# Kernel optimization log

Hardware: AMD Instinct MI355X
Metric: run time of the kernel (lower is better)

The kernel has to match this reference:

```python
import jax, jax.numpy as jnp
import numpy as np

D = 32       # hidden_size (hardcoded in AR.__init__)
H = 16       # num_heads
HD = D // H  # head_dim = 2
L = 8        # num DiT blocks
MLP = 128    # mlp_ratio 4.0
B, S, T, P = 16, 1024, 256, 32
SCALE = float(1.0 / np.sqrt(HD))


def _ln(x, g, b, eps=1e-6):
    mu = jnp.mean(x, axis=-1, keepdims=True)
    var = jnp.mean((x - mu) ** 2, axis=-1, keepdims=True)
    return (x - mu) * jax.lax.rsqrt(var + eps) * g + b


def _mha(q_in, kv_in, in_w, in_b, out_w, out_b):
    # nn.MultiheadAttention math, batch-first layout (permutation-equivalent)
    wq, wk, wv = in_w[:D], in_w[D:2 * D], in_w[2 * D:]
    bq, bk, bv = in_b[:D], in_b[D:2 * D], in_b[2 * D:]
    Bq, Sq = q_in.shape[0], q_in.shape[1]
    Sk = kv_in.shape[1]
    q = (q_in @ wq.T + bq).reshape(Bq, Sq, H, HD)
    k = (kv_in @ wk.T + bk).reshape(Bq, Sk, H, HD)
    v = (kv_in @ wv.T + bv).reshape(Bq, Sk, H, HD)
    scores = jnp.einsum('bqhd,bkhd->bhqk', q, k) * SCALE
    a = jax.nn.softmax(scores, axis=-1)
    o = jnp.einsum('bhqk,bkhd->bqhd', a, v).reshape(Bq, Sq, D)
    return o @ out_w.T + out_b


def setup_inputs() -> dict:
    key = jax.random.key(0)
    ks = iter(jax.random.split(key, 40))
    rn = lambda k, sh, sc=1.0: jax.random.normal(k, sh, jnp.float32) * sc
    inp = {
        'x': rn(next(ks), (B, S, D)),
        'speaker_emb': rn(next(ks), (B, P, D)),
        'text_phonemes': rn(next(ks), (B, T, D)),
        'timestep_emb': rn(next(ks), (B, D)),
        'mask': jnp.ones((S,), jnp.float32),
        # per-block params, stacked over L for lax.scan
        'ln1_g': jnp.ones((L, D)), 'ln1_b': jnp.zeros((L, D)),
        'ln2_g': jnp.ones((L, D)), 'ln2_b': jnp.zeros((L, D)),
        'ln22_g': jnp.ones((L, D)), 'ln22_b': jnp.zeros((L, D)),
        'ln3_g': jnp.ones((L, D)), 'ln3_b': jnp.zeros((L, D)),
        'attn_in_w': rn(next(ks), (L, 3 * D, D), 0.1), 'attn_in_b': jnp.zeros((L, 3 * D)),
        'attn_out_w': rn(next(ks), (L, D, D), 0.1), 'attn_out_b': jnp.zeros((L, D)),
        'cross_in_w': rn(next(ks), (L, 3 * D, D), 0.1), 'cross_in_b': jnp.zeros((L, 3 * D)),
        'cross_out_w': rn(next(ks), (L, D, D), 0.1), 'cross_out_b': jnp.zeros((L, D)),
        'ts_w': rn(next(ks), (L, 2 * D, D), 0.1), 'ts_b': jnp.zeros((L, 2 * D)),
        'fc1_w': rn(next(ks), (L, MLP, D), 0.1), 'fc1_b': jnp.zeros((L, MLP)),
        'fc2_w': rn(next(ks), (L, D, MLP), 0.1), 'fc2_b': jnp.zeros((L, D)),
    }
    return inp


def _forward(x, speaker_emb, text_phonemes, timestep_emb, mask, params):
    m = mask[None, :, None]  # (1, S, 1), matches mask.unsqueeze(0).unsqueeze(2)
    def body(h, p):
        h = h * m
        hn = _ln(h, p['ln1_g'], p['ln1_b'])
        h = h + _mha(hn, hn, p['attn_in_w'], p['attn_in_b'], p['attn_out_w'], p['attn_out_b'])
        # both cross attentions use cross_attn weights (cross_attn2 is dead code in source)
        ca1 = _mha(_ln(h, p['ln2_g'], p['ln2_b']), text_phonemes,
                   p['cross_in_w'], p['cross_in_b'], p['cross_out_w'], p['cross_out_b'])
        ca2 = _mha(_ln(h, p['ln22_g'], p['ln22_b']), speaker_emb,
                   p['cross_in_w'], p['cross_in_b'], p['cross_out_w'], p['cross_out_b'])
        h = h + ca1 + ca2
        ss = timestep_emb @ p['ts_w'].T + p['ts_b']        # (B, 2D)
        scale, shift = ss[:, :D], ss[:, D:]
        hm = _ln(h, p['ln3_g'], p['ln3_b']) * (1.0 + scale[:, None, :]) + shift[:, None, :]
        mlp = jax.nn.gelu(hm @ p['fc1_w'].T + p['fc1_b'], approximate=False) @ p['fc2_w'].T + p['fc2_b']
        return (h + mlp) * m, None
    out, _ = jax.lax.scan(body, x, params)
    return out


def reference(x, speaker_emb, text_phonemes, timestep_emb, mask,
              ln1_g, ln1_b, ln2_g, ln2_b, ln22_g, ln22_b, ln3_g, ln3_b,
              attn_in_w, attn_in_b, attn_out_w, attn_out_b,
              cross_in_w, cross_in_b, cross_out_w, cross_out_b,
              ts_w, ts_b, fc1_w, fc1_b, fc2_w, fc2_b):
    params = dict(ln1_g=ln1_g, ln1_b=ln1_b, ln2_g=ln2_g, ln2_b=ln2_b,
                  ln22_g=ln22_g, ln22_b=ln22_b, ln3_g=ln3_g, ln3_b=ln3_b,
                  attn_in_w=attn_in_w, attn_in_b=attn_in_b,
                  attn_out_w=attn_out_w, attn_out_b=attn_out_b,
                  cross_in_w=cross_in_w, cross_in_b=cross_in_b,
                  cross_out_w=cross_out_w, cross_out_b=cross_out_b,
                  ts_w=ts_w, ts_b=ts_b, fc1_w=fc1_w, fc1_b=fc1_b,
                  fc2_w=fc2_w, fc2_b=fc2_b)
    return _forward(x, speaker_emb, text_phonemes, timestep_emb, mask, params)
```

## Files before the change

kernel.cpp:

```cpp
#include <hip/hip_runtime.h>
#include <math.h>

#define NB 16
#define SEQ 1024
#define NT 16384
#define TT 256
#define PP 32
#define NL 8
#define SCALE 0.70710678118654752f
#define LOG2E 1.4426950408889634f
#define CS (SCALE * LOG2E)

static __device__ __forceinline__ float exp2fast(float x) {
#if __has_builtin(__builtin_amdgcn_exp2f)
  return __builtin_amdgcn_exp2f(x);
#else
  return exp2f(x);
#endif
}

__global__ __launch_bounds__(256) void k_pre(const float* __restrict__ tse,
                                             const float* __restrict__ tsw,
                                             const float* __restrict__ tsb,
                                             float* __restrict__ ssa,
                                             const float* __restrict__ text,
                                             const float* __restrict__ spk,
                                             const float* __restrict__ cw,
                                             const float* __restrict__ cb,
                                             float* __restrict__ kvtT,
                                             float* __restrict__ kvsT) {
  __shared__ float sh[64 * 33];
  int tid = threadIdx.x;
  int bx = blockIdx.x;
  if (bx < 32) {
    int idx = bx * 256 + tid;
    int l = idx >> 10;
    int rem = idx & 1023;
    int b = rem >> 6;
    int j = rem & 63;
    const float* wr = tsw + ((size_t)l * 64 + j) * 32;
    const float* xr = tse + b * 32;
    float acc = tsb[l * 64 + j];
#pragma unroll
    for (int e = 0; e < 32; e++) acc = fmaf(xr[e], wr[e], acc);
    ssa[idx] = acc;
    return;
  }
  const float* src;
  float* dst;
  int l, tok0, ntok;
  if (bx < 544) {
    l = (bx - 32) >> 6; tok0 = ((bx - 32) & 63) * 64; ntok = NB * TT; src = text;
    dst = kvtT + (size_t)l * 64 * ntok;
  } else {
    l = (bx - 544) >> 3; tok0 = ((bx - 544) & 7) * 64; ntok = NB * PP; src = spk;
    dst = kvsT + (size_t)l * 64 * ntok;
  }
  const float* w = cw + (size_t)l * 96 * 32 + 32 * 32;
  const float* wb = cb + (size_t)l * 96 + 32;
  for (int i = tid; i < 64 * 32; i += 256) {
    int tl = i >> 5, e = i & 31;
    sh[tl * 33 + e] = src[(size_t)(tok0 + tl) * 32 + e];
  }
  __syncthreads();
  int tl = tid & 63;
  int wv = tid >> 6;
#pragma unroll
  for (int k = 0; k < 16; k++) {
    int j = __builtin_amdgcn_readfirstlane(wv + 4 * k);
    const float* wr = w + j * 32;
    const float* hr = sh + tl * 33;
    float acc = wb[j];
#pragma unroll
    for (int e = 0; e < 32; e++) acc = fmaf(hr[e], wr[e], acc);
    dst[(size_t)j * ntok + tok0 + tl] = acc;
  }
}

__device__ __forceinline__ void load_row32(const float* __restrict__ base, int tok, float* r) {
#pragma unroll
  for (int e = 0; e < 32; e++) r[e] = base[(size_t)e * NT + tok];
}

__device__ __forceinline__ void ln_core(float* r) {
  float a0 = 0, a1 = 0, a2 = 0, a3 = 0;
#pragma unroll
  for (int e = 0; e < 32; e += 4) { a0 += r[e]; a1 += r[e + 1]; a2 += r[e + 2]; a3 += r[e + 3]; }
  float mu = ((a0 + a1) + (a2 + a3)) * (1.0f / 32.0f);
  float v0 = 0, v1 = 0, v2 = 0, v3 = 0;
#pragma unroll
  for (int e = 0; e < 32; e += 4) {
    float d0 = r[e] - mu, d1 = r[e + 1] - mu, d2 = r[e + 2] - mu, d3 = r[e + 3] - mu;
    v0 = fmaf(d0, d0, v0); v1 = fmaf(d1, d1, v1); v2 = fmaf(d2, d2, v2); v3 = fmaf(d3, d3, v3);
  }
  float rstd = rsqrtf(((v0 + v1) + (v2 + v3)) * (1.0f / 32.0f) + 1e-6f);
#pragma unroll
  for (int e = 0; e < 32; e++) r[e] = (r[e] - mu) * rstd;
}

__global__ __launch_bounds__(256) void k_qkv(const float* __restrict__ hin,
                                             int rowmajor,
                                             float* __restrict__ hT,
                                             const float* __restrict__ mask,
                                             const float* __restrict__ w,
                                             const float* __restrict__ wb,
                                             const float* __restrict__ g,
                                             const float* __restrict__ bv,
                                             float* __restrict__ qkvT) {
  int tid = threadIdx.x;
  int tok0 = blockIdx.x * 64;
  int yc = blockIdx.y;
  int tl = tid & 63, wv = tid >> 6;
  int tok = tok0 + tl;
  float r[32];
  if (rowmajor) {
    float m = mask[tok & (SEQ - 1)];
#pragma unroll
    for (int e = 0; e < 32; e++) r[e] = hin[(size_t)tok * 32 + e] * m;
    if (yc == 0 && wv == 0) {
#pragma unroll
      for (int e = 0; e < 32; e++) hT[(size_t)e * NT + tok] = r[e];
    }
  } else {
    load_row32(hin, tok, r);
  }
  ln_core(r);
#pragma unroll
  for (int e = 0; e < 32; e++) r[e] = fmaf(r[e], g[e], bv[e]);
#pragma unroll
  for (int k = 0; k < 6; k++) {
    int j = __builtin_amdgcn_readfirstlane(yc * 24 + wv + 4 * k);
    const float* wr = w + j * 32;
    float acc = wb[j];
#pragma unroll
    for (int e = 0; e < 32; e++) acc = fmaf(r[e], wr[e], acc);
    qkvT[(size_t)j * NT + tok] = acc;
  }
}

__global__ __launch_bounds__(256) void k_projq12(const float* __restrict__ hA,
                                                 const float* __restrict__ oT,
                                                 const float* __restrict__ aow,
                                                 const float* __restrict__ aob,
                                                 float* __restrict__ hB,
                                                 const float* __restrict__ cwq,
                                                 const float* __restrict__ cbq,
                                                 const float* __restrict__ g2, const float* __restrict__ b2,
                                                 const float* __restrict__ g22, const float* __restrict__ b22,
                                                 float* __restrict__ q1T,
                                                 float* __restrict__ q2T) {
  __shared__ float sh[32 * 33];
  __shared__ float so[32 * 33];
  int tid = threadIdx.x;
  int tok0 = blockIdx.x * 32;
  int y = blockIdx.y;
  for (int i = tid; i < 1024; i += 256) {
    int e = i >> 5, t = i & 31;
    sh[t * 33 + e] = hA[(size_t)e * NT + tok0 + t];
    so[t * 33 + e] = oT[(size_t)e * NT + tok0 + t];
  }
  __syncthreads();
  int tl = tid & 31, jg = tid >> 5;
#pragma unroll
  for (int kk = 0; kk < 4; kk++) {
    int j = jg + 8 * kk;
    const float* wr = aow + j * 32;
    float acc = aob[j];
#pragma unroll
    for (int i = 0; i < 32; i++) acc = fmaf(so[tl * 33 + i], wr[i], acc);
    float hp = sh[tl * 33 + j] + acc;
    sh[tl * 33 + j] = hp;
    if (y == 0) hB[(size_t)j * NT + tok0 + tl] = hp;
  }
  __syncthreads();
  float r[32];
#pragma unroll
  for (int i = 0; i < 32; i++) r[i] = sh[tl * 33 + i];
  ln_core(r);
  const float* g = y ? g22 : g2;
  const float* bb = y ? b22 : b2;
  float* dst = y ? q2T : q1T;
#pragma unroll
  for (int i = 0; i < 32; i++) r[i] = fmaf(r[i], g[i], bb[i]);
#pragma unroll
  for (int kk = 0; kk < 4; kk++) {
    int j = jg + 8 * kk;
    const float* wr = cwq + j * 32;
    float acc = cbq[j];
#pragma unroll
    for (int i = 0; i < 32; i++) acc = fmaf(r[i], wr[i], acc);
    dst[(size_t)j * NT + tok0 + tl] = acc;
  }
}

__global__ __launch_bounds__(256) void k_projfc1(const float* __restrict__ hBp,
                                                 const float* __restrict__ o1T,
                                                 const float* __restrict__ o2T,
                                                 const float* __restrict__ cow,
                                                 const float* __restrict__ cob,
                                                 float* __restrict__ hC,
                                                 const float* __restrict__ ssl,
                                                 const float* __restrict__ g3, const float* __restrict__ b3,
                                                 const float* __restrict__ w1, const float* __restrict__ b1,
                                                 float* __restrict__ uT) {
  __shared__ float sh[32 * 33];
  __shared__ float so[32 * 33];
  int tid = threadIdx.x;
  int tok0 = blockIdx.x * 32;
  int yc = blockIdx.y;
  for (int i = tid; i < 1024; i += 256) {
    int e = i >> 5, t = i & 31;
    sh[t * 33 + e] = hBp[(size_t)e * NT + tok0 + t];
    so[t * 33 + e] = o1T[(size_t)e * NT + tok0 + t] + o2T[(size_t)e * NT + tok0 + t];
  }
  __syncthreads();
  int tl = tid & 31, jg = tid >> 5;
#pragma unroll
  for (int kk = 0; kk < 4; kk++) {
    int j = jg + 8 * kk;
    const float* wr = cow + j * 32;
    float acc = 2.0f * cob[j];
#pragma unroll
    for (int i = 0; i < 32; i++) acc = fmaf(so[tl * 33 + i], wr[i], acc);
    float hp = sh[tl * 33 + j] + acc;
    sh[tl * 33 + j] = hp;
    if (yc == 0) hC[(size_t)j * NT + tok0 + tl] = hp;
  }
  __syncthreads();
  float r[32];
#pragma unroll
  for (int i = 0; i < 32; i++) r[i] = sh[tl * 33 + i];
  ln_core(r);
  int b = tok0 >> 10;
  const float* sc = ssl + b * 64;
#pragma unroll
  for (int i = 0; i < 32; i++) {
    float ln = fmaf(r[i], g3[i], b3[i]);
    r[i] = fmaf(ln, 1.0f + sc[i], sc[32 + i]);
  }
#pragma unroll
  for (int kk = 0; kk < 4; kk++) {
    int j = yc * 32 + jg + 8 * kk;
    const float* wr = w1 + j * 32;
    float acc = b1[j];
#pragma unroll
    for (int i = 0; i < 32; i++) acc = fmaf(r[i], wr[i], acc);
    float ge = 0.5f * acc * (1.0f + erff(acc * 0.70710678118654752f));
    uT[(size_t)j * NT + tok0 + tl] = ge;
  }
}

template <int SK, int SETS>
__device__ __forceinline__ void attn_core(const float* __restrict__ qb,
                                          const float* __restrict__ kb,
                                          const float* __restrict__ vb,
                                          int kvld,
                                          float* __restrict__ ob) {
  constexpr int RPW = 4 * SETS;
  constexpr int RPB = 4 * RPW;
  constexpr int NRC = SEQ / RPB;
  int tid = threadIdx.x;
  int bx = blockIdx.x;
  int rc = bx % NRC, bh = bx / NRC;
  int b = bh >> 4, hh = bh & 15;
  int wv = tid >> 6, lane = tid & 63;
  int rg = lane >> 4, kl = lane & 15;
  int rbase = rc * RPB + wv * RPW + rg;

  const float* qxp = qb + (size_t)(2 * hh) * NT + b * SEQ;
  const float* qyp = qxp + NT;
  const float* kx = kb + (size_t)(2 * hh) * kvld + b * SK;
  const float* ky = kx + kvld;
  const float* vx = vb + (size_t)(2 * hh) * kvld + b * SK;
  const float* vy = vx + kvld;

  float qx[SETS], qy[SETS], sum[SETS], ox[SETS], oy[SETS];
#pragma unroll
  for (int s = 0; s < SETS; s++) {
    qx[s] = qxp[rbase + 4 * s] * CS;
    qy[s] = qyp[rbase + 4 * s] * CS;
    sum[s] = 0.f; ox[s] = 0.f; oy[s] = 0.f;
  }

  if constexpr (SK >= 64) {
    const float4* kx4 = (const float4*)(kx + kl * 4);
    const float4* ky4 = (const float4*)(ky + kl * 4);
    const float4* vx4 = (const float4*)(vx + kl * 4);
    const float4* vy4 = (const float4*)(vy + kl * 4);
#pragma unroll 4
    for (int c = 0; c < SK / 64; c++) {
      float4 k4x = kx4[c * 16];
      float4 k4y = ky4[c * 16];
      float4 v4x = vx4[c * 16];
      float4 v4y = vy4[c * 16];
#pragma unroll
      for (int s = 0; s < SETS; s++) {
        float e0 = exp2fast(fmaf(qy[s], k4y.x, qx[s] * k4x.x));
        float e1 = exp2fast(fmaf(qy[s], k4y.y, qx[s] * k4x.y));
        float e2 = exp2fast(fmaf(qy[s], k4y.z, qx[s] * k4x.z));
        float e3 = exp2fast(fmaf(qy[s], k4y.w, qx[s] * k4x.w));
        sum[s] += (e0 + e1) + (e2 + e3);
        ox[s] = fmaf(e0, v4x.x, ox[s]);
        ox[s] = fmaf(e1, v4x.y, ox[s]);
        ox[s] = fmaf(e2, v4x.z, ox[s]);
        ox[s] = fmaf(e3, v4x.w, ox[s]);
        oy[s] = fmaf(e0, v4y.x, oy[s]);
        oy[s] = fmaf(e1, v4y.y, oy[s]);
        oy[s] = fmaf(e2, v4y.z, oy[s]);
        oy[s] = fmaf(e3, v4y.w, oy[s]);
      }
    }
  } else {
    float2 k2x = *(const float2*)(kx + kl * 2);
    float2 k2y = *(const float2*)(ky + kl * 2);
    float2 v2x = *(const float2*)(vx + kl * 2);
    float2 v2y = *(const float2*)(vy + kl * 2);
#pragma unroll
    for (int s = 0; s < SETS; s++) {
      float e0 = exp2fast(fmaf(qy[s], k2y.x, qx[s] * k2x.x));
      float e1 = exp2fast(fmaf(qy[s], k2y.y, qx[s] * k2x.y));
      sum[s] += e0 + e1;
      ox[s] = fmaf(e0, v2x.x, ox[s]);
      ox[s] = fmaf(e1, v2x.y, ox[s]);
      oy[s] = fmaf(e0, v2y.x, oy[s]);
      oy[s] = fmaf(e1, v2y.y, oy[s]);
    }
  }

  float* oxr = ob + (size_t)(2 * hh) * NT + b * SEQ;
  float* oyr = oxr + NT;
#pragma unroll
  for (int s = 0; s < SETS; s++) {
    float sm = sum[s];
    float o1 = ox[s];
    float o2 = oy[s];
#pragma unroll
    for (int off = 1; off < 16; off <<= 1) {
      sm += __shfl_xor(sm, off);
      o1 += __shfl_xor(o1, off);
      o2 += __shfl_xor(o2, off);
    }
    if (kl == 0) {
      float inv = 1.0f / sm;
      int r = rbase + 4 * s;
      oxr[r] = o1 * inv;
      oyr[r] = o2 * inv;
    }
  }
}

__global__ __launch_bounds__(256) void k_attn_self(const float* __restrict__ qkvT,
                                                   float* __restrict__ oT) {
  attn_core<SEQ, 8>(qkvT, qkvT + (size_t)32 * NT, qkvT + (size_t)64 * NT, NT, oT);
}

__global__ __launch_bounds__(256) void k_attn_cross(const float* __restrict__ q1T,
                                                    const float* __restrict__ q2T,
                                                    const float* __restrict__ kvt,
                                                    const float* __restrict__ kvs,
                                                    float* __restrict__ o1T,
                                                    float* __restrict__ o2T) {
  if (blockIdx.y == 0)
    attn_core<TT, 8>(q1T, kvt, kvt + (size_t)32 * (NB * TT), NB * TT, o1T);
  else
    attn_core<PP, 8>(q2T, kvs, kvs + (size_t)32 * (NB * PP), NB * PP, o2T);
}

__global__ __launch_bounds__(256) void k_fc2(const float* __restrict__ uT,
                                             float* hT,
                                             float* __restrict__ out_rm,
                                             const float* __restrict__ mask,
                                             const float* __restrict__ w2,
                                             const float* __restrict__ b2) {
  __shared__ __align__(16) float shu[64 * 132];
  int tid = threadIdx.x;
  int tok0 = blockIdx.x * 64, yc = blockIdx.y;
  for (int i = tid; i < 64 * 128; i += 256) {
    int e = i >> 6, tl = i & 63;
    shu[tl * 132 + e] = uT[(size_t)e * NT + tok0 + tl];
  }
  __syncthreads();
  int tl = tid & 63, wv = tid >> 6;
  int tok = tok0 + tl;
  int j0 = __builtin_amdgcn_readfirstlane(yc * 16 + wv);
  int j1 = __builtin_amdgcn_readfirstlane(j0 + 4);
  int j2 = __builtin_amdgcn_readfirstlane(j0 + 8);
  int j3 = __builtin_amdgcn_readfirstlane(j0 + 12);
  const float* w0 = w2 + j0 * 128;
  const float* w1 = w2 + j1 * 128;
  const float* w2r = w2 + j2 * 128;
  const float* w3 = w2 + j3 * 128;
  float a0 = b2[j0], a1 = b2[j1], a2 = b2[j2], a3 = b2[j3];
  const float4* ur = (const float4*)(shu + tl * 132);
#pragma unroll
  for (int m = 0; m < 32; m++) {
    float4 t = ur[m];
    a0 = fmaf(t.x, w0[4 * m], a0); a0 = fmaf(t.y, w0[4 * m + 1], a0);
    a0 = fmaf(t.z, w0[4 * m + 2], a0); a0 = fmaf(t.w, w0[4 * m + 3], a0);
    a1 = fmaf(t.x, w1[4 * m], a1); a1 = fmaf(t.y, w1[4 * m + 1], a1);
    a1 = fmaf(t.z, w1[4 * m + 2], a1); a1 = fmaf(t.w, w1[4 * m + 3], a1);
    a2 = fmaf(t.x, w2r[4 * m], a2); a2 = fmaf(t.y, w2r[4 * m + 1], a2);
    a2 = fmaf(t.z, w2r[4 * m + 2], a2); a2 = fmaf(t.w, w2r[4 * m + 3], a2);
    a3 = fmaf(t.x, w3[4 * m], a3); a3 = fmaf(t.y, w3[4 * m + 1], a3);
    a3 = fmaf(t.z, w3[4 * m + 2], a3); a3 = fmaf(t.w, w3[4 * m + 3], a3);
  }
  float mk = mask[tok & (SEQ - 1)];
  size_t g0 = (size_t)j0 * NT + tok, g1 = (size_t)j1 * NT + tok;
  size_t g2i = (size_t)j2 * NT + tok, g3 = (size_t)j3 * NT + tok;
  float r0 = (hT[g0] + a0) * mk;
  float r1 = (hT[g1] + a1) * mk;
  float r2 = (hT[g2i] + a2) * mk;
  float r3 = (hT[g3] + a3) * mk;
  if (out_rm) {
    out_rm[(size_t)tok * 32 + j0] = r0;
    out_rm[(size_t)tok * 32 + j1] = r1;
    out_rm[(size_t)tok * 32 + j2] = r2;
    out_rm[(size_t)tok * 32 + j3] = r3;
  } else {
    hT[g0] = r0;
    hT[g1] = r1;
    hT[g2i] = r2;
    hT[g3] = r3;
  }
}

extern "C" void kernel_launch(void* const* d_in, const int* in_sizes, int n_in,
                              void* d_out, int out_size, void* d_ws, size_t ws_size,
                              hipStream_t stream) {
  const float* x = (const float*)d_in[0];
  const float* spk = (const float*)d_in[1];
  const float* text = (const float*)d_in[2];
  const float* tse = (const float*)d_in[3];
  const float* mask = (const float*)d_in[4];
  const float* ln1_g = (const float*)d_in[5];
  const float* ln1_b = (const float*)d_in[6];
  const float* ln2_g = (const float*)d_in[7];
  const float* ln2_b = (const float*)d_in[8];
  const float* ln22_g = (const float*)d_in[9];
  const float* ln22_b = (const float*)d_in[10];
  const float* ln3_g = (const float*)d_in[11];
  const float* ln3_b = (const float*)d_in[12];
  const float* aw = (const float*)d_in[13];
  const float* ab = (const float*)d_in[14];
  const float* aow = (const float*)d_in[15];
  const float* aob = (const float*)d_in[16];
  const float* cw = (const float*)d_in[17];
  const float* cb = (const float*)d_in[18];
  const float* cow = (const float*)d_in[19];
  const float* cob = (const float*)d_in[20];
  const float* tsw = (const float*)d_in[21];
  const float* tsb = (const float*)d_in[22];
  const float* f1w = (const float*)d_in[23];
  const float* f1b = (const float*)d_in[24];
  const float* f2w = (const float*)d_in[25];
  const float* f2b = (const float*)d_in[26];

  float* ws = (float*)d_ws;
  const size_t SL = (size_t)32 * NT;
  float* hS = ws;
  float* qkvT = ws + SL;
  float* q1T = ws + 2 * SL;
  float* q2T = ws + 3 * SL;
  float* oS = ws + 4 * SL;
  float* hB = ws + SL;
  float* o1c = ws + 6 * SL;
  float* o2c = ws + 7 * SL;
  float* uT = ws + 2 * SL;
  float* kvtT = ws + 8 * SL;
  float* kvsT = kvtT + (size_t)NL * 64 * (NB * TT);
  float* ssa = kvsT + (size_t)NL * 64 * (NB * PP);

  k_pre<<<608, 256, 0, stream>>>(tse, tsw, tsb, ssa, text, spk, cw, cb, kvtT, kvsT);

  for (int l = 0; l < NL; l++) {
    k_qkv<<<dim3(256, 4), 256, 0, stream>>>((l == 0) ? x : hS, (l == 0) ? 1 : 0, hS, mask,
                                            aw + (size_t)l * 96 * 32, ab + l * 96,
                                            ln1_g + l * 32, ln1_b + l * 32, qkvT);
    k_attn_self<<<2048, 256, 0, stream>>>(qkvT, oS);
    k_projq12<<<dim3(512, 2), 256, 0, stream>>>(hS, oS,
                                                aow + (size_t)l * 32 * 32, aob + l * 32, hB,
                                                cw + (size_t)l * 96 * 32, cb + l * 96,
                                                ln2_g + l * 32, ln2_b + l * 32,
                                                ln22_g + l * 32, ln22_b + l * 32, q1T, q2T);
    k_attn_cross<<<dim3(2048, 2), 256, 0, stream>>>(q1T, q2T,
                                                    kvtT + (size_t)l * 64 * (NB * TT),
                                                    kvsT + (size_t)l * 64 * (NB * PP),
                                                    o1c, o2c);
    k_projfc1<<<dim3(512, 4), 256, 0, stream>>>(hB, o1c, o2c,
                                                cow + (size_t)l * 32 * 32, cob + l * 32, hS,
                                                ssa + (size_t)l * NB * 64,
                                                ln3_g + l * 32, ln3_b + l * 32,
                                                f1w + (size_t)l * 128 * 32, f1b + l * 128, uT);
    k_fc2<<<dim3(256, 2), 256, 0, stream>>>(uT, hS, (l == NL - 1) ? (float*)d_out : nullptr,
                                            mask, f2w + (size_t)l * 32 * 128, f2b + l * 32);
  }
}
```

Measured before the change: 1.063 ms.

## Switch projection kernels to one-thread-per-token and halve attention rows per wave

The projection kernels (projq12, projfc1, fc2) now use 64-thread blocks where each thread owns one token's full row in registers. This replaces the shared-memory transpose and the split of output columns across waves, removing LDS traffic and syncs. Each thread now does redundant weight loads and far more FMAs, and the grids are much smaller. Attention SETS drops from 8 to 4, doubling the grids, and the workspace buffers are reassigned so hS no longer aliases with other buffers.

```diff
diff --git a/kernel.cpp b/kernel.cpp
--- a/kernel.cpp
+++ b/kernel.cpp
@@ -138,115 +138,126 @@
   }
 }
 
-__global__ __launch_bounds__(256) void k_projq12(const float* __restrict__ hA,
-                                                 const float* __restrict__ oT,
-                                                 const float* __restrict__ aow,
-                                                 const float* __restrict__ aob,
-                                                 float* __restrict__ hB,
-                                                 const float* __restrict__ cwq,
-                                                 const float* __restrict__ cbq,
-                                                 const float* __restrict__ g2, const float* __restrict__ b2,
-                                                 const float* __restrict__ g22, const float* __restrict__ b22,
-                                                 float* __restrict__ q1T,
-                                                 float* __restrict__ q2T) {
-  __shared__ float sh[32 * 33];
-  __shared__ float so[32 * 33];
-  int tid = threadIdx.x;
-  int tok0 = blockIdx.x * 32;
+__global__ __launch_bounds__(64) void k_projq12(const float* __restrict__ hA,
+                                                const float* __restrict__ oT,
+                                                const float* __restrict__ aow,
+                                                const float* __restrict__ aob,
+                                                float* __restrict__ hB,
+                                                const float* __restrict__ cwq,
+                                                const float* __restrict__ cbq,
+                                                const float* __restrict__ g2, const float* __restrict__ b2,
+                                                const float* __restrict__ g22, const float* __restrict__ b22,
+                                                float* __restrict__ q1T,
+                                                float* __restrict__ q2T) {
+  int tok = blockIdx.x * 64 + threadIdx.x;
   int y = blockIdx.y;
-  for (int i = tid; i < 1024; i += 256) {
-    int e = i >> 5, t = i & 31;
-    sh[t * 33 + e] = hA[(size_t)e * NT + tok0 + t];
-    so[t * 33 + e] = oT[(size_t)e * NT + tok0 + t];
-  }
-  __syncthreads();
-  int tl = tid & 31, jg = tid >> 5;
-#pragma unroll
-  for (int kk = 0; kk < 4; kk++) {
-    int j = jg + 8 * kk;
+  float o[32], h[32];
+  load_row32(oT, tok, o);
+  load_row32(hA, tok, h);
+#pragma unroll
+  for (int j = 0; j < 32; j++) {
     const float* wr = aow + j * 32;
     float acc = aob[j];
 #pragma unroll
-    for (int i = 0; i < 32; i++) acc = fmaf(so[tl * 33 + i], wr[i], acc);
-    float hp = sh[tl * 33 + j] + acc;
-    sh[tl * 33 + j] = hp;
-    if (y == 0) hB[(size_t)j * NT + tok0 + tl] = hp;
-  }
-  __syncthreads();
-  float r[32];
-#pragma unroll
-  for (int i = 0; i < 32; i++) r[i] = sh[tl * 33 + i];
-  ln_core(r);
+    for (int i = 0; i < 32; i++) acc = fmaf(o[i], wr[i], acc);
+    h[j] += acc;
+  }
+  if (y == 0) {
+#pragma unroll
+    for (int j = 0; j < 32; j++) hB[(size_t)j * NT + tok] = h[j];
+  }
+  ln_core(h);
   const float* g = y ? g22 : g2;
   const float* bb = y ? b22 : b2;
   float* dst = y ? q2T : q1T;
 #pragma unroll
-  for (int i = 0; i < 32; i++) r[i] = fmaf(r[i], g[i], bb[i]);
-#pragma unroll
-  for (int kk = 0; kk < 4; kk++) {
-    int j = jg + 8 * kk;
+  for (int i = 0; i < 32; i++) h[i] = fmaf(h[i], g[i], bb[i]);
+#pragma unroll
+  for (int j = 0; j < 32; j++) {
     const float* wr = cwq + j * 32;
     float acc = cbq[j];
 #pragma unroll
-    for (int i = 0; i < 32; i++) acc = fmaf(r[i], wr[i], acc);
-    dst[(size_t)j * NT + tok0 + tl] = acc;
-  }
-}
-
-__global__ __launch_bounds__(256) void k_projfc1(const float* __restrict__ hBp,
-                                                 const float* __restrict__ o1T,
-                                                 const float* __restrict__ o2T,
-                                                 const float* __restrict__ cow,
-                                                 const float* __restrict__ cob,
-                                                 float* __restrict__ hC,
-                                                 const float* __restrict__ ssl,
-                                                 const float* __restrict__ g3, const float* __restrict__ b3,
-                                                 const float* __restrict__ w1, const float* __restrict__ b1,
-                                                 float* __restrict__ uT) {
-  __shared__ float sh[32 * 33];
-  __shared__ float so[32 * 33];
-  int tid = threadIdx.x;
-  int tok0 = blockIdx.x * 32;
+    for (int i = 0; i < 32; i++) acc = fmaf(h[i], wr[i], acc);
+    dst[(size_t)j * NT + tok] = acc;
+  }
+}
+
+__global__ __launch_bounds__(64) void k_projfc1(const float* __restrict__ hBp,
+                                                const float* __restrict__ o1T,
+                                                const float* __restrict__ o2T,
+                                                const float* __restrict__ cow,
+                                                const float* __restrict__ cob,
+                                                float* __restrict__ hC,
+                                                const float* __restrict__ ssl,
+                                                const float* __restrict__ g3, const float* __restrict__ b3,
+                                                const float* __restrict__ w1, const float* __restrict__ b1,
+                                                float* __restrict__ uT) {
+  int tok = blockIdx.x * 64 + threadIdx.x;
   int yc = blockIdx.y;
-  for (int i = tid; i < 1024; i += 256) {
-    int e = i >> 5, t = i & 31;
-    sh[t * 33 + e] = hBp[(size_t)e * NT + tok0 + t];
-    so[t * 33 + e] = o1T[(size_t)e * NT + tok0 + t] + o2T[(size_t)e * NT + tok0 + t];
-  }
-  __syncthreads();
-  int tl = tid & 31, jg = tid >> 5;
-#pragma unroll
-  for (int kk = 0; kk < 4; kk++) {
-    int j = jg + 8 * kk;
+  float o[32], h[32];
+#pragma unroll
+  for (int e = 0; e < 32; e++)
+    o[e] = o1T[(size_t)e * NT + tok] + o2T[(size_t)e * NT + tok];
+  load_row32(hBp, tok, h);
+#pragma unroll
+  for (int j = 0; j < 32; j++) {
     const float* wr = cow + j * 32;
     float acc = 2.0f * cob[j];
 #pragma unroll
-    for (int i = 0; i < 32; i++) acc = fmaf(so[tl * 33 + i], wr[i], acc);
-    float hp = sh[tl * 33 + j] + acc;
-    sh[tl * 33 + j] = hp;
-    if (yc == 0) hC[(size_t)j * NT + tok0 + tl] = hp;
-  }
-  __syncthreads();
-  float r[32];
-#pragma unroll
-  for (int i = 0; i < 32; i++) r[i] = sh[tl * 33 + i];
-  ln_core(r);
-  int b = tok0 >> 10;
+    for (int i = 0; i < 32; i++) acc = fmaf(o[i], wr[i], acc);
+    h[j] += acc;
+  }
+  if (yc == 0) {
+#pragma unroll
+    for (int j = 0; j < 32; j++) hC[(size_t)j * NT + tok] = h[j];
+  }
+  ln_core(h);
+  int b = tok >> 10;
   const float* sc = ssl + b * 64;
 #pragma unroll
   for (int i = 0; i < 32; i++) {
-    float ln = fmaf(r[i], g3[i], b3[i]);
-    r[i] = fmaf(ln, 1.0f + sc[i], sc[32 + i]);
-  }
-#pragma unroll
-  for (int kk = 0; kk < 4; kk++) {
-    int j = yc * 32 + jg + 8 * kk;
+    float ln = fmaf(h[i], g3[i], b3[i]);
+    h[i] = fmaf(ln, 1.0f + sc[i], sc[32 + i]);
+  }
+#pragma unroll
+  for (int k = 0; k < 32; k++) {
+    int j = yc * 32 + k;
     const float* wr = w1 + j * 32;
     float acc = b1[j];
 #pragma unroll
-    for (int i = 0; i < 32; i++) acc = fmaf(r[i], wr[i], acc);
+    for (int i = 0; i < 32; i++) acc = fmaf(h[i], wr[i], acc);
     float ge = 0.5f * acc * (1.0f + erff(acc * 0.70710678118654752f));
-    uT[(size_t)j * NT + tok0 + tl] = ge;
+    uT[(size_t)j * NT + tok] = ge;
+  }
+}
+
+__global__ __launch_bounds__(64) void k_fc2(const float* __restrict__ uT,
+                                            float* hC,
+                                            float* __restrict__ out_rm,
+                                            const float* __restrict__ mask,
+                                            const float* __restrict__ w2,
+                                            const float* __restrict__ b2) {
+  int tok = blockIdx.x * 64 + threadIdx.x;
+  int yc = blockIdx.y;
+  int j0 = yc * 8;
+  float acc[8];
+#pragma unroll
+  for (int k = 0; k < 8; k++) acc[k] = b2[j0 + k];
+#pragma unroll
+  for (int e = 0; e < 128; e++) {
+    float u = uT[(size_t)e * NT + tok];
+#pragma unroll
+    for (int k = 0; k < 8; k++) acc[k] = fmaf(u, w2[(j0 + k) * 128 + e], acc[k]);
+  }
+  float mk = mask[tok & (SEQ - 1)];
+#pragma unroll
+  for (int k = 0; k < 8; k++) {
+    size_t gi = (size_t)(j0 + k) * NT + tok;
+    float r = (hC[gi] + acc[k]) * mk;
+    if (out_rm)
+      out_rm[(size_t)tok * 32 + j0 + k] = r;
+    else
+      hC[gi] = r;
   }
 }
 
@@ -283,16 +294,13 @@
   }
 
   if constexpr (SK >= 64) {
-    const float4* kx4 = (const float4*)(kx + kl * 4);
-    const float4* ky4 = (const float4*)(ky + kl * 4);
-    const float4* vx4 = (const float4*)(vx + kl * 4);
-    const float4* vy4 = (const float4*)(vy + kl * 4);
 #pragma unroll 4
     for (int c = 0; c < SK / 64; c++) {
-      float4 k4x = kx4[c * 16];
-      float4 k4y = ky4[c * 16];
-      float4 v4x = vx4[c * 16];
-      float4 v4y = vy4[c * 16];
+      int o = c * 64 + kl * 4;
+      float4 k4x = *(const float4*)(kx + o);
+      float4 k4y = *(const float4*)(ky + o);
+      float4 v4x = *(const float4*)(vx + o);
+      float4 v4y = *(const float4*)(vy + o);
 #pragma unroll
       for (int s = 0; s < SETS; s++) {
         float e0 = exp2fast(fmaf(qy[s], k4y.x, qx[s] * k4x.x));
@@ -351,7 +359,7 @@
 
 __global__ __launch_bounds__(256) void k_attn_self(const float* __restrict__ qkvT,
                                                    float* __restrict__ oT) {
-  attn_core<SEQ, 8>(qkvT, qkvT + (size_t)32 * NT, qkvT + (size_t)64 * NT, NT, oT);
+  attn_core<SEQ, 4>(qkvT, qkvT + (size_t)32 * NT, qkvT + (size_t)64 * NT, NT, oT);
 }
 
 __global__ __launch_bounds__(256) void k_attn_cross(const float* __restrict__ q1T,
@@ -361,67 +369,9 @@
                                                     float* __restrict__ o1T,
                                                     float* __restrict__ o2T) {
   if (blockIdx.y == 0)
-    attn_core<TT, 8>(q1T, kvt, kvt + (size_t)32 * (NB * TT), NB * TT, o1T);
+    attn_core<TT, 4>(q1T, kvt, kvt + (size_t)32 * (NB * TT), NB * TT, o1T);
   else
-    attn_core<PP, 8>(q2T, kvs, kvs + (size_t)32 * (NB * PP), NB * PP, o2T);
-}
-
-__global__ __launch_bounds__(256) void k_fc2(const float* __restrict__ uT,
-                                             float* hT,
-                                             float* __restrict__ out_rm,
-                                             const float* __restrict__ mask,
-                                             const float* __restrict__ w2,
-                                             const float* __restrict__ b2) {
-  __shared__ __align__(16) float shu[64 * 132];
-  int tid = threadIdx.x;
-  int tok0 = blockIdx.x * 64, yc = blockIdx.y;
-  for (int i = tid; i < 64 * 128; i += 256) {
-    int e = i >> 6, tl = i & 63;
-    shu[tl * 132 + e] = uT[(size_t)e * NT + tok0 + tl];
-  }
-  __syncthreads();
-  int tl = tid & 63, wv = tid >> 6;
-  int tok = tok0 + tl;
-  int j0 = __builtin_amdgcn_readfirstlane(yc * 16 + wv);
-  int j1 = __builtin_amdgcn_readfirstlane(j0 + 4);
-  int j2 = __builtin_amdgcn_readfirstlane(j0 + 8);
-  int j3 = __builtin_amdgcn_readfirstlane(j0 + 12);
-  const float* w0 = w2 + j0 * 128;
-  const float* w1 = w2 + j1 * 128;
-  const float* w2r = w2 + j2 * 128;
-  const float* w3 = w2 + j3 * 128;
-  float a0 = b2[j0], a1 = b2[j1], a2 = b2[j2], a3 = b2[j3];
-  const float4* ur = (const float4*)(shu + tl * 132);
-#pragma unroll
-  for (int m = 0; m < 32; m++) {
-    float4 t = ur[m];
-    a0 = fmaf(t.x, w0[4 * m], a0); a0 = fmaf(t.y, w0[4 * m + 1], a0);
-    a0 = fmaf(t.z, w0[4 * m + 2], a0); a0 = fmaf(t.w, w0[4 * m + 3], a0);
-    a1 = fmaf(t.x, w1[4 * m], a1); a1 = fmaf(t.y, w1[4 * m + 1], a1);
-    a1 = fmaf(t.z, w1[4 * m + 2], a1); a1 = fmaf(t.w, w1[4 * m + 3], a1);
-    a2 = fmaf(t.x, w2r[4 * m], a2); a2 = fmaf(t.y, w2r[4 * m + 1], a2);
-    a2 = fmaf(t.z, w2r[4 * m + 2], a2); a2 = fmaf(t.w, w2r[4 * m + 3], a2);
-    a3 = fmaf(t.x, w3[4 * m], a3); a3 = fmaf(t.y, w3[4 * m + 1], a3);
-    a3 = fmaf(t.z, w3[4 * m + 2], a3); a3 = fmaf(t.w, w3[4 * m + 3], a3);
-  }
-  float mk = mask[tok & (SEQ - 1)];
-  size_t g0 = (size_t)j0 * NT + tok, g1 = (size_t)j1 * NT + tok;
-  size_t g2i = (size_t)j2 * NT + tok, g3 = (size_t)j3 * NT + tok;
-  float r0 = (hT[g0] + a0) * mk;
-  float r1 = (hT[g1] + a1) * mk;
-  float r2 = (hT[g2i] + a2) * mk;
-  float r3 = (hT[g3] + a3) * mk;
-  if (out_rm) {
-    out_rm[(size_t)tok * 32 + j0] = r0;
-    out_rm[(size_t)tok * 32 + j1] = r1;
-    out_rm[(size_t)tok * 32 + j2] = r2;
-    out_rm[(size_t)tok * 32 + j3] = r3;
-  } else {
-    hT[g0] = r0;
-    hT[g1] = r1;
-    hT[g2i] = r2;
-    hT[g3] = r3;
-  }
+    attn_core<PP, 4>(q2T, kvs, kvs + (size_t)32 * (NB * PP), NB * PP, o2T);
 }
 
 extern "C" void kernel_launch(void* const* d_in, const int* in_sizes, int n_in,
@@ -457,15 +407,22 @@
 
   float* ws = (float*)d_ws;
   const size_t SL = (size_t)32 * NT;
-  float* hS = ws;
-  float* qkvT = ws + SL;
-  float* q1T = ws + 2 * SL;
-  float* q2T = ws + 3 * SL;
-  float* oS = ws + 4 * SL;
-  float* hB = ws + SL;
-  float* o1c = ws + 6 * SL;
-  float* o2c = ws + 7 * SL;
-  float* uT = ws + 2 * SL;
+  float* S0 = ws;
+  float* S1 = ws + SL;
+  float* S2 = ws + 2 * SL;
+  float* S4 = ws + 4 * SL;
+  float* S5 = ws + 5 * SL;
+  float* S6 = ws + 6 * SL;
+  float* S7 = ws + 7 * SL;
+  float* qkvT = S1;
+  float* oS = S0;
+  float* q1T = S1;
+  float* q2T = S2;
+  float* hS = S4;
+  float* hB = S5;
+  float* o1c = S6;
+  float* o2c = S7;
+  float* uT = S0;
   float* kvtT = ws + 8 * SL;
   float* kvsT = kvtT + (size_t)NL * 64 * (NB * TT);
   float* ssa = kvsT + (size_t)NL * 64 * (NB * PP);
@@ -476,22 +433,22 @@
     k_qkv<<<dim3(256, 4), 256, 0, stream>>>((l == 0) ? x : hS, (l == 0) ? 1 : 0, hS, mask,
                                             aw + (size_t)l * 96 * 32, ab + l * 96,
                                             ln1_g + l * 32, ln1_b + l * 32, qkvT);
-    k_attn_self<<<2048, 256, 0, stream>>>(qkvT, oS);
-    k_projq12<<<dim3(512, 2), 256, 0, stream>>>(hS, oS,
-                                                aow + (size_t)l * 32 * 32, aob + l * 32, hB,
-                                                cw + (size_t)l * 96 * 32, cb + l * 96,
-                                                ln2_g + l * 32, ln2_b + l * 32,
-                                                ln22_g + l * 32, ln22_b + l * 32, q1T, q2T);
-    k_attn_cross<<<dim3(2048, 2), 256, 0, stream>>>(q1T, q2T,
+    k_attn_self<<<4096, 256, 0, stream>>>(qkvT, oS);
+    k_projq12<<<dim3(256, 2), 64, 0, stream>>>(hS, oS,
+                                               aow + (size_t)l * 32 * 32, aob + l * 32, hB,
+                                               cw + (size_t)l * 96 * 32, cb + l * 96,
+                                               ln2_g + l * 32, ln2_b + l * 32,
+                                               ln22_g + l * 32, ln22_b + l * 32, q1T, q2T);
+    k_attn_cross<<<dim3(4096, 2), 256, 0, stream>>>(q1T, q2T,
                                                     kvtT + (size_t)l * 64 * (NB * TT),
                                                     kvsT + (size_t)l * 64 * (NB * PP),
                                                     o1c, o2c);
-    k_projfc1<<<dim3(512, 4), 256, 0, stream>>>(hB, o1c, o2c,
-                                                cow + (size_t)l * 32 * 32, cob + l * 32, hS,
-                                                ssa + (size_t)l * NB * 64,
-                                                ln3_g + l * 32, ln3_b + l * 32,
-                                                f1w + (size_t)l * 128 * 32, f1b + l * 128, uT);
-    k_fc2<<<dim3(256, 2), 256, 0, stream>>>(uT, hS, (l == NL - 1) ? (float*)d_out : nullptr,
-                                            mask, f2w + (size_t)l * 32 * 128, f2b + l * 32);
-  }
-}
+    k_projfc1<<<dim3(256, 4), 64, 0, stream>>>(hB, o1c, o2c,
+                                               cow + (size_t)l * 32 * 32, cob + l * 32, hS,
+                                               ssa + (size_t)l * NB * 64,
+                                               ln3_g + l * 32, ln3_b + l * 32,
+                                               f1w + (size_t)l * 128 * 32, f1b + l * 128, uT);
+    k_fc2<<<dim3(256, 4), 64, 0, stream>>>(uT, hS, (l == NL - 1) ? (float*)d_out : nullptr,
+                                           mask, f2w + (size_t)l * 32 * 128, f2b + l * 32);
+  }
+}
```

New measurement: 1.540 ms. 44.9% more time.
